# Kernel optimization log

Hardware: AMD Instinct MI355X
Metric: run time of the kernel (lower is better)

Reference implementation:

```python
import jax, jax.numpy as jnp
import numpy as np

D = 256; NH = 8; HD = D // NH; L = 4; P = 4; NQ = 900; BS = 8; DFFN = 1024
SHAPES = np.array([[128, 128], [64, 64], [32, 32], [16, 16]])  # (H, W) per level, static metadata
NV = int((SHAPES[:, 0] * SHAPES[:, 1]).sum())
EPS = 1e-6


def setup_inputs():
    key = jax.random.key(0)
    ks = iter(jax.random.split(key, 48))

    def nrm(shape, scale=0.02):
        return jax.random.normal(next(ks), shape, jnp.float32) * scale

    lsi = np.concatenate([[0], np.cumsum(SHAPES[:, 0] * SHAPES[:, 1])[:-1]]).astype(np.int64)
    return {
        'tgt': nrm((NQ, BS, D), 1.0),
        'tgt_query_pos': nrm((NQ, BS, D), 1.0),
        'tgt_reference_points': jax.random.uniform(next(ks), (NQ, BS, L, 2), jnp.float32),
        'memory': nrm((NV, BS, D), 1.0),
        'memory_spatial_shapes': jnp.asarray(SHAPES, jnp.int32),
        'memory_level_start_index': jnp.asarray(lsi, jnp.int32),
        'w_norm_sa': jnp.ones((D,), jnp.float32),
        'w_norm_ca': jnp.ones((D,), jnp.float32),
        'w_norm_ffn': jnp.ones((D,), jnp.float32),
        'ls_sa': jnp.full((D,), 1e-4, jnp.float32),
        'ls_ca': jnp.full((D,), 1e-4, jnp.float32),
        'ls_ffn': jnp.full((D,), 1e-4, jnp.float32),
        'Wq': nrm((D, D)), 'Wk': nrm((D, D)), 'Wv': nrm((D, D)),
        'bq': jnp.zeros((D,), jnp.float32), 'bk': jnp.zeros((D,), jnp.float32), 'bv': jnp.zeros((D,), jnp.float32),
        'Wo_sa': nrm((D, D)), 'bo_sa': jnp.zeros((D,), jnp.float32),
        'Wv_proj': nrm((D, D)), 'bv_proj': jnp.zeros((D,), jnp.float32),
        'W_off': nrm((NH * L * P * 2, D)), 'b_off': nrm((NH * L * P * 2,), 0.1),
        'W_attn': nrm((NH * L * P, D)), 'b_attn': jnp.zeros((NH * L * P,), jnp.float32),
        'W_out_ca': nrm((D, D)), 'bo_ca': jnp.zeros((D,), jnp.float32),
        'Wg': nrm((DFFN, D)), 'bg': jnp.zeros((DFFN,), jnp.float32),
        'Wu': nrm((DFFN, D)), 'bu': jnp.zeros((DFFN,), jnp.float32),
        'Wf': nrm((D, DFFN)), 'bf': jnp.zeros((D,), jnp.float32),
    }


def rmsnorm(x, w):
    return x * jax.lax.rsqrt(jnp.mean(x * x, axis=-1, keepdims=True) + EPS) * w


def ms_deform_sample(v, loc, attw):
    # v: (bs, nv, NH, HD); loc: (bs, nq, NH, L, P, 2) normalized (x, y); attw: (bs, nq, NH, L, P)
    bs, nq = loc.shape[0], loc.shape[1]
    out = jnp.zeros((bs, nq, NH, HD), loc.dtype)
    b_idx = jnp.arange(bs)[:, None, None, None]
    h_idx = jnp.arange(NH)[None, None, :, None]
    start = 0
    for l in range(L):
        Hl, Wl = int(SHAPES[l, 0]), int(SHAPES[l, 1])
        vf = v[:, start:start + Hl * Wl]  # (bs, Hl*Wl, NH, HD)
        start += Hl * Wl
        # grid_sample(align_corners=False, padding=zeros) pixel mapping
        x = loc[:, :, :, l, :, 0] * Wl - 0.5
        y = loc[:, :, :, l, :, 1] * Hl - 0.5
        x0 = jnp.floor(x)
        y0 = jnp.floor(y)
        acc = jnp.zeros((bs, nq, NH, P, HD), loc.dtype)
        for dx in (0, 1):
            for dy in (0, 1):
                xi = x0 + dx
                yi = y0 + dy
                w = (1.0 - jnp.abs(x - xi)) * (1.0 - jnp.abs(y - yi))
                valid = (xi >= 0) & (xi <= Wl - 1) & (yi >= 0) & (yi <= Hl - 1)
                w = jnp.where(valid, w, 0.0)
                idx = (jnp.clip(yi, 0, Hl - 1) * Wl + jnp.clip(xi, 0, Wl - 1)).astype(jnp.int32)
                acc = acc + w[..., None] * vf[b_idx, idx, h_idx]  # (bs, nq, NH, P, HD)
        out = out + jnp.einsum('bqhp,bqhpd->bqhd', attw[:, :, :, l], acc)
    return out


def reference(tgt, tgt_query_pos, tgt_reference_points, memory, memory_spatial_shapes,
              memory_level_start_index, w_norm_sa, w_norm_ca, w_norm_ffn, ls_sa, ls_ca, ls_ffn,
              Wq, Wk, Wv, bq, bk, bv, Wo_sa, bo_sa, Wv_proj, bv_proj, W_off, b_off, W_attn,
              b_attn, W_out_ca, bo_ca, Wg, bg, Wu, bu, Wf, bf):
    nq, bs, d = tgt.shape
    # --- self-attention (pre-norm + LayerScale residual) ---
    xn = rmsnorm(tgt, w_norm_sa)
    qk = xn + tgt_query_pos
    q = (qk @ Wq.T + bq).reshape(nq, bs, NH, HD)
    k = (qk @ Wk.T + bk).reshape(nq, bs, NH, HD)
    vv = (xn @ Wv.T + bv).reshape(nq, bs, NH, HD)
    scores = jnp.einsum('qbhd,kbhd->bhqk', q, k) * (1.0 / np.sqrt(HD))
    attn = jax.nn.softmax(scores, axis=-1)
    sa = jnp.einsum('bhqk,kbhd->qbhd', attn, vv).reshape(nq, bs, d) @ Wo_sa.T + bo_sa
    tgt = tgt + ls_sa * sa
    # --- multi-scale deformable cross-attention (identity=zeros in original) ---
    xn = rmsnorm(tgt, w_norm_ca)
    qca = jnp.swapaxes(xn + tgt_query_pos, 0, 1)  # (bs, nq, d)
    val = (jnp.swapaxes(memory, 0, 1) @ Wv_proj.T + bv_proj).reshape(bs, -1, NH, HD)
    off = (qca @ W_off.T + b_off).reshape(bs, nq, NH, L, P, 2)
    attw = jax.nn.softmax((qca @ W_attn.T + b_attn).reshape(bs, nq, NH, L * P), axis=-1)
    attw = attw.reshape(bs, nq, NH, L, P)
    norm = jnp.asarray(SHAPES[:, ::-1].copy(), jnp.float32)  # (W, H) per level
    ref = jnp.swapaxes(tgt_reference_points, 0, 1)  # (bs, nq, L, 2)
    loc = ref[:, :, None, :, None, :] + off / norm[None, None, None, :, None, :]
    ca = ms_deform_sample(val, loc, attw).reshape(bs, nq, d) @ W_out_ca.T + bo_ca
    tgt = tgt + ls_ca * jnp.swapaxes(ca, 0, 1)
    # --- SwiGLU FFN ---
    xn = rmsnorm(tgt, w_norm_ffn)
    ffn = (jax.nn.silu(xn @ Wg.T + bg) * (xn @ Wu.T + bu)) @ Wf.T + bf
    return tgt + ls_ffn * ffn
```

## Files before the change

kernel.cpp:

```cpp
#include <hip/hip_runtime.h>

typedef unsigned short ushort_t;
typedef unsigned int uint32;
typedef __bf16 bf16x8 __attribute__((ext_vector_type(8)));
typedef float f32x4 __attribute__((ext_vector_type(4)));
typedef ushort_t us4 __attribute__((ext_vector_type(4)));

#define D_    256
#define NH_   8
#define HD_   32
#define NQ_   900
#define BS_   8
#define TOK_  7200
#define NV_   21760
#define QP_   928
#define DFFN_ 1024

__device__ __forceinline__ ushort_t f2bf(float x) {
    union { float f; uint32 u; } v; v.f = x;
    uint32 r = v.u + 0x7FFFu + ((v.u >> 16) & 1u);
    return (ushort_t)(r >> 16);
}
__device__ __forceinline__ float bf2f(ushort_t h) {
    union { uint32 u; float f; } v; v.u = ((uint32)h) << 16;
    return v.f;
}
__device__ __forceinline__ int imin(int a, int b) { return a < b ? a : b; }
__device__ __forceinline__ int imax(int a, int b) { return a > b ? a : b; }

__global__ __launch_bounds__(256) void cvtall_k(
    const float* __restrict__ s0, const float* __restrict__ s1, const float* __restrict__ s2,
    const float* __restrict__ s3, const float* __restrict__ s4, const float* __restrict__ s5,
    const float* __restrict__ s6, const float* __restrict__ s7, const float* __restrict__ s8,
    const float* __restrict__ s9, const float* __restrict__ s10, ushort_t* __restrict__ dst,
    const float* __restrict__ bq, const float* __restrict__ bk,
    const float* __restrict__ boff, const float* __restrict__ battn,
    float* __restrict__ bias_qk, float* __restrict__ bias_ol) {
    int tid = threadIdx.x;
    if (blockIdx.x == 0) {
        bias_qk[tid] = bq[tid];
        bias_qk[256 + tid] = bk[tid];
        bias_ol[tid] = boff[tid];
        if (tid < 128) bias_ol[256 + tid] = battn[tid];
    }
    int id = blockIdx.x * 256 + tid;
    const float* s; int off;
    if      (id <  16384) { s = s0;  off = id; }
    else if (id <  32768) { s = s1;  off = id - 16384; }
    else if (id <  49152) { s = s2;  off = id - 32768; }
    else if (id <  65536) { s = s3;  off = id - 49152; }
    else if (id <  81920) { s = s4;  off = id - 65536; }
    else if (id <  98304) { s = s5;  off = id - 81920; }
    else if (id < 114688) { s = s6;  off = id - 98304; }
    else if (id < 122880) { s = s7;  off = id - 114688; }
    else if (id < 188416) { s = s8;  off = id - 122880; }
    else if (id < 253952) { s = s9;  off = id - 188416; }
    else                  { s = s10; off = id - 253952; }
    f32x4 v = *(const f32x4*)(s + (size_t)off * 4);
    us4 t;
#pragma unroll
    for (int e = 0; e < 4; e++) t[e] = f2bf(v[e]);
    *(us4*)(dst + (size_t)id * 4) = t;
}

__global__ __launch_bounds__(256) void rms_k(const float* __restrict__ x,
                                             const float* __restrict__ pos,
                                             const float* __restrict__ wn,
                                             ushort_t* __restrict__ xn_out,
                                             ushort_t* __restrict__ qk_out) {
    int r = blockIdx.x, tid = threadIdx.x;
    float v = x[r * D_ + tid];
    float ss = v * v;
#pragma unroll
    for (int o = 32; o; o >>= 1) ss += __shfl_xor(ss, o, 64);
    __shared__ float part[4];
    if ((tid & 63) == 0) part[tid >> 6] = ss;
    __syncthreads();
    float tot = part[0] + part[1] + part[2] + part[3];
    float sc = rsqrtf(tot * (1.f / 256.f) + 1e-6f);
    float xn = v * sc * wn[tid];
    if (xn_out) xn_out[r * D_ + tid] = f2bf(xn);
    if (qk_out) qk_out[r * D_ + tid] = f2bf(xn + pos[r * D_ + tid]);
}

enum { EPI_RESID, EPI_QK2, EPI_VT, EPI_VAL, EPI_OFFLOG };

template <int EPI, bool AF32, int BM, int BN, int WGM, int WGN, int TK>
__global__ __launch_bounds__(WGM * WGN * 64) void gemm2_k(
    const void* __restrict__ Ap, const ushort_t* __restrict__ Wp,
    const float* __restrict__ bias, void* __restrict__ outp, void* __restrict__ outp2,
    int M, int N, int swz,
    const float* __restrict__ resid, const float* __restrict__ ls, float scale) {
    constexpr int THREADS = WGM * WGN * 64;
    constexpr int NK  = TK / 32;
    constexpr int LDK = 40;
    constexpr int WR  = BM / WGM, WC = BN / WGN;
    constexpr int FM  = WR / 16,  FN = WC / 16;
    constexpr int ACH = AF32 ? (BM * 32 / 4 / THREADS) : (BM * 32 / 8 / THREADS);
    constexpr int BCH = BN * 32 / 8 / THREADS;

    __shared__ __align__(16) ushort_t As[2][BM * LDK];
    __shared__ __align__(16) ushort_t Bs[2][BN * LDK];

    const int tid = threadIdx.x, l = tid & 63, w = tid >> 6;
    const int wm = w % WGM, wn = w / WGM;
    int by = blockIdx.y;
    if (swz) { int cpx = gridDim.y >> 3; by = (by & 7) * cpx + (by >> 3); }
    const int m0 = by * BM, n0 = blockIdx.x * BN;
    const int lr = l & 15, lkb = (l >> 4) * 8;

    const ushort_t* Ab = (const ushort_t*)Ap;
    const float*    Af = (const float*)Ap;

    int aRow[ACH], aK[ACH], bRow[BCH], bK[BCH];
#pragma unroll
    for (int ch = 0; ch < ACH; ch++) {
        int cid = ch * THREADS + tid;
        if constexpr (AF32) { aRow[ch] = cid >> 3; aK[ch] = (cid & 7) * 4; }
        else                { aRow[ch] = cid >> 2; aK[ch] = (cid & 3) * 8; }
    }
#pragma unroll
    for (int ch = 0; ch < BCH; ch++) {
        int cid = ch * THREADS + tid;
        bRow[ch] = cid >> 2; bK[ch] = (cid & 3) * 8;
    }
    int aGRow[ACH];
#pragma unroll
    for (int ch = 0; ch < ACH; ch++) aGRow[ch] = imin(m0 + aRow[ch], M - 1);

    f32x4  aSTf[AF32 ? ACH : 1];
    bf16x8 aSTb[AF32 ? 1 : ACH];
    bf16x8 bST[BCH];

    auto load_regs = [&](int kt) {
        const int k0 = kt * 32;
#pragma unroll
        for (int ch = 0; ch < ACH; ch++) {
            if constexpr (AF32)
                aSTf[ch] = *(const f32x4*)(Af + (size_t)aGRow[ch] * TK + k0 + aK[ch]);
            else
                aSTb[ch] = *(const bf16x8*)(Ab + (size_t)aGRow[ch] * TK + k0 + aK[ch]);
        }
#pragma unroll
        for (int ch = 0; ch < BCH; ch++)
            bST[ch] = *(const bf16x8*)(Wp + (size_t)(n0 + bRow[ch]) * TK + k0 + bK[ch]);
    };
    auto write_lds = [&](int buf) {
#pragma unroll
        for (int ch = 0; ch < ACH; ch++) {
            if constexpr (AF32) {
                us4 t;
#pragma unroll
                for (int e = 0; e < 4; e++) t[e] = f2bf(aSTf[ch][e]);
                *(us4*)&As[buf][aRow[ch] * LDK + aK[ch]] = t;
            } else {
                *(bf16x8*)&As[buf][aRow[ch] * LDK + aK[ch]] = aSTb[ch];
            }
        }
#pragma unroll
        for (int ch = 0; ch < BCH; ch++)
            *(bf16x8*)&Bs[buf][bRow[ch] * LDK + bK[ch]] = bST[ch];
    };

    f32x4 acc[FM][FN];
#pragma unroll
    for (int i = 0; i < FM; i++)
#pragma unroll
        for (int j = 0; j < FN; j++) acc[i][j] = f32x4{0.f, 0.f, 0.f, 0.f};

    load_regs(0);
    write_lds(0);
    __syncthreads();

    for (int kt = 0; kt < NK; ++kt) {
        const int c = kt & 1;
        if (kt + 1 < NK) load_regs(kt + 1);

        bf16x8 af[FM], bf_[FN];
#pragma unroll
        for (int i = 0; i < FM; i++)
            af[i] = *(const bf16x8*)&As[c][(wm * WR + i * 16 + lr) * LDK + lkb];
#pragma unroll
        for (int j = 0; j < FN; j++)
            bf_[j] = *(const bf16x8*)&Bs[c][(wn * WC + j * 16 + lr) * LDK + lkb];
#pragma unroll
        for (int i = 0; i < FM; i++)
#pragma unroll
            for (int j = 0; j < FN; j++)
                acc[i][j] = __builtin_amdgcn_mfma_f32_16x16x32_bf16(af[i], bf_[j], acc[i][j], 0, 0, 0);

        if (kt + 1 < NK) write_lds(c ^ 1);
        __syncthreads();
    }

#pragma unroll
    for (int i = 0; i < FM; i++)
#pragma unroll
        for (int j = 0; j < FN; j++) {
            int col = n0 + wn * WC + j * 16 + lr;
            float bvv = bias[col];
#pragma unroll
            for (int e = 0; e < 4; e++) {
                int row = m0 + wm * WR + i * 16 + (l >> 4) * 4 + e;
                if (row >= M) continue;
                float v = acc[i][j][e] + bvv;
                if constexpr (EPI == EPI_RESID) {
                    size_t idx = (size_t)row * N + col;
                    ((float*)outp)[idx] = resid[idx] + ls[col] * v;
                } else if constexpr (EPI == EPI_QK2) {
                    int c2 = col & 255;
                    int q = row >> 3, bb = row & 7, h = c2 >> 5, hd = c2 & 31;
                    ushort_t* dst = (col < 256) ? (ushort_t*)outp : (ushort_t*)outp2;
                    float sc = (col < 256) ? scale : 1.f;
                    dst[((bb * NH_ + h) * QP_ + q) * HD_ + hd] = f2bf(v * sc);
                } else if constexpr (EPI == EPI_VT) {
                    int q = row >> 3, bb = row & 7, h = col >> 5, hd = col & 31;
                    ((ushort_t*)outp)[((bb * NH_ + h) * HD_ + hd) * QP_ + q] = f2bf(v);
                } else if constexpr (EPI == EPI_VAL) {
                    int vv = row >> 3, bb = row & 7, h = col >> 5, d = col & 31;
                    ((ushort_t*)outp)[(((size_t)(bb * NH_ + h)) * NV_ + vv) * HD_ + d] = f2bf(v);
                } else if constexpr (EPI == EPI_OFFLOG) {
                    if (col < 256) ((float*)outp)[(size_t)row * 256 + col] = v;
                    else           ((float*)outp2)[(size_t)row * 128 + col - 256] = v;
                }
            }
        }
}

__global__ __launch_bounds__(256) void ffn_k(
    const ushort_t* __restrict__ Ap, const ushort_t* __restrict__ Wg,
    const ushort_t* __restrict__ Wu, const float* __restrict__ bgp,
    const float* __restrict__ bup, ushort_t* __restrict__ outp, int M) {
    constexpr int BM = 64, BN = 128, TK = 256, NK = TK / 32, LDK = 40;
    constexpr int WR = 32, WC = 64, FM = 2, FN = 4;

    __shared__ __align__(16) ushort_t As[2][BM * LDK];
    __shared__ __align__(16) ushort_t Gs[2][BN * LDK];
    __shared__ __align__(16) ushort_t Us[2][BN * LDK];

    const int tid = threadIdx.x, l = tid & 63, w = tid >> 6;
    const int wm = w & 1, wn = w >> 1;
    const int m0 = blockIdx.y * BM, n0 = blockIdx.x * BN;
    const int lr = l & 15, lkb = (l >> 4) * 8;

    const int aRow = tid >> 2, aK = (tid & 3) * 8;
    int bRow[2], bK[2];
#pragma unroll
    for (int ch = 0; ch < 2; ch++) { int cid = ch * 256 + tid; bRow[ch] = cid >> 2; bK[ch] = (cid & 3) * 8; }
    const int aGRow = imin(m0 + aRow, M - 1);

    bf16x8 aST, gST[2], uST[2];
    auto load_regs = [&](int kt) {
        const int k0 = kt * 32;
        aST = *(const bf16x8*)(Ap + (size_t)aGRow * TK + k0 + aK);
#pragma unroll
        for (int ch = 0; ch < 2; ch++) {
            gST[ch] = *(const bf16x8*)(Wg + (size_t)(n0 + bRow[ch]) * TK + k0 + bK[ch]);
            uST[ch] = *(const bf16x8*)(Wu + (size_t)(n0 + bRow[ch]) * TK + k0 + bK[ch]);
        }
    };
    auto write_lds = [&](int buf) {
        *(bf16x8*)&As[buf][aRow * LDK + aK] = aST;
#pragma unroll
        for (int ch = 0; ch < 2; ch++) {
            *(bf16x8*)&Gs[buf][bRow[ch] * LDK + bK[ch]] = gST[ch];
            *(bf16x8*)&Us[buf][bRow[ch] * LDK + bK[ch]] = uST[ch];
        }
    };

    f32x4 accG[FM][FN], accU[FM][FN];
#pragma unroll
    for (int i = 0; i < FM; i++)
#pragma unroll
        for (int j = 0; j < FN; j++) { accG[i][j] = f32x4{0,0,0,0}; accU[i][j] = f32x4{0,0,0,0}; }

    load_regs(0);
    write_lds(0);
    __syncthreads();

    for (int kt = 0; kt < NK; ++kt) {
        const int c = kt & 1;
        if (kt + 1 < NK) load_regs(kt + 1);
        bf16x8 af[FM], gf[FN], uf[FN];
#pragma unroll
        for (int i = 0; i < FM; i++)
            af[i] = *(const bf16x8*)&As[c][(wm * WR + i * 16 + lr) * LDK + lkb];
#pragma unroll
        for (int j = 0; j < FN; j++) {
            gf[j] = *(const bf16x8*)&Gs[c][(wn * WC + j * 16 + lr) * LDK + lkb];
            uf[j] = *(const bf16x8*)&Us[c][(wn * WC + j * 16 + lr) * LDK + lkb];
        }
#pragma unroll
        for (int i = 0; i < FM; i++)
#pragma unroll
            for (int j = 0; j < FN; j++) {
                accG[i][j] = __builtin_amdgcn_mfma_f32_16x16x32_bf16(af[i], gf[j], accG[i][j], 0, 0, 0);
                accU[i][j] = __builtin_amdgcn_mfma_f32_16x16x32_bf16(af[i], uf[j], accU[i][j], 0, 0, 0);
            }
        if (kt + 1 < NK) write_lds(c ^ 1);
        __syncthreads();
    }

#pragma unroll
    for (int i = 0; i < FM; i++)
#pragma unroll
        for (int j = 0; j < FN; j++) {
            int col = n0 + wn * WC + j * 16 + lr;
            float bg_ = bgp[col], bu_ = bup[col];
#pragma unroll
            for (int e = 0; e < 4; e++) {
                int row = m0 + wm * WR + i * 16 + (l >> 4) * 4 + e;
                if (row >= M) continue;
                float g = accG[i][j][e] + bg_;
                float u = accU[i][j][e] + bu_;
                float s = g / (1.f + __expf(-g));
                outp[(size_t)row * DFFN_ + col] = f2bf(s * u);
            }
        }
}

__global__ __launch_bounds__(256) void attn2_k(const ushort_t* __restrict__ qb,
                                               const ushort_t* __restrict__ kb,
                                               const ushort_t* __restrict__ vtb,
                                               ushort_t* __restrict__ sab) {
    __shared__ __align__(16) ushort_t Pl[4][16 * 40];
    const int tid = threadIdx.x, l = tid & 63, w = tid >> 6;
    const int bh = blockIdx.y, b = bh >> 3, h = bh & 7;
    const int q0 = (blockIdx.x * 4 + w) * 16;
    if (q0 >= NQ_) return;
    const int q = l & 15, g = l >> 4;
    ushort_t* Pw = &Pl[w][0];

    const bf16x8 qf = *(const bf16x8*)(qb + ((size_t)bh * QP_ + q0 + q) * HD_ + g * 8);
    const ushort_t* kbase = kb + (size_t)bh * QP_ * HD_;
    const ushort_t* vbase = vtb + (size_t)bh * HD_ * QP_;

    f32x4 O0 = {0.f, 0.f, 0.f, 0.f}, O1 = {0.f, 0.f, 0.f, 0.f};
    float m = -1e30f, sl = 0.f;

    auto ldk = [&](int t, int u) {
        return *(const bf16x8*)(kbase + (size_t)(t * 32 + u * 16 + q) * HD_ + g * 8);
    };
    auto ldv = [&](int t, int dh) {
        return *(const bf16x8*)(vbase + (size_t)(dh * 16 + q) * QP_ + t * 32 + g * 8);
    };
    bf16x8 kA = ldk(0, 0), kB = ldk(0, 1), v0 = ldv(0, 0), v1 = ldv(0, 1);

    for (int t = 0; t < 29; ++t) {
        bf16x8 nkA, nkB, nv0, nv1;
        if (t < 28) { nkA = ldk(t + 1, 0); nkB = ldk(t + 1, 1); nv0 = ldv(t + 1, 0); nv1 = ldv(t + 1, 1); }
        const f32x4 z = {0.f, 0.f, 0.f, 0.f};
        f32x4 sA = __builtin_amdgcn_mfma_f32_16x16x32_bf16(kA, qf, z, 0, 0, 0);
        f32x4 sB = __builtin_amdgcn_mfma_f32_16x16x32_bf16(kB, qf, z, 0, 0, 0);
        if (t == 28) {
            int k0 = 896 + g * 4;
#pragma unroll
            for (int e = 0; e < 4; e++) {
                if (k0 + e >= NQ_)      sA[e] = -1e30f;
                if (k0 + 16 + e >= NQ_) sB[e] = -1e30f;
            }
        }
        float tm = fmaxf(fmaxf(fmaxf(sA[0], sA[1]), fmaxf(sA[2], sA[3])),
                         fmaxf(fmaxf(sB[0], sB[1]), fmaxf(sB[2], sB[3])));
        tm = fmaxf(tm, __shfl_xor(tm, 16, 64));
        tm = fmaxf(tm, __shfl_xor(tm, 32, 64));
        float mn = fmaxf(m, tm);
        float r = exp2f(m - mn);
        m = mn;
#pragma unroll
        for (int e = 0; e < 4; e++) { O0[e] *= r; O1[e] *= r; }
        float pA[4], pB[4], ps = 0.f;
#pragma unroll
        for (int e = 0; e < 4; e++) {
            pA[e] = exp2f(sA[e] - m); pB[e] = exp2f(sB[e] - m);
            ps += pA[e] + pB[e];
        }
        sl = sl * r + ps;
        uint32 a0, a1, b0, b1;
        asm("v_cvt_pk_bf16_f32 %0, %1, %2" : "=v"(a0) : "v"(pA[0]), "v"(pA[1]));
        asm("v_cvt_pk_bf16_f32 %0, %1, %2" : "=v"(a1) : "v"(pA[2]), "v"(pA[3]));
        asm("v_cvt_pk_bf16_f32 %0, %1, %2" : "=v"(b0) : "v"(pB[0]), "v"(pB[1]));
        asm("v_cvt_pk_bf16_f32 %0, %1, %2" : "=v"(b1) : "v"(pB[2]), "v"(pB[3]));
        { uint2 tt; tt.x = a0; tt.y = a1; *(uint2*)(Pw + q * 40 + g * 4) = tt; }
        { uint2 tt; tt.x = b0; tt.y = b1; *(uint2*)(Pw + q * 40 + 16 + g * 4) = tt; }
        bf16x8 pf = *(const bf16x8*)(Pw + q * 40 + g * 8);
        O0 = __builtin_amdgcn_mfma_f32_16x16x32_bf16(v0, pf, O0, 0, 0, 0);
        O1 = __builtin_amdgcn_mfma_f32_16x16x32_bf16(v1, pf, O1, 0, 0, 0);
        kA = nkA; kB = nkB; v0 = nv0; v1 = nv1;
    }

    sl += __shfl_xor(sl, 16, 64);
    sl += __shfl_xor(sl, 32, 64);
    float inv = 1.f / sl;
    int row_q = q0 + q;
    if (row_q < NQ_) {
        ushort_t* op = sab + ((size_t)row_q * BS_ + b) * D_ + h * HD_ + g * 4;
#pragma unroll
        for (int dh = 0; dh < 2; dh++) {
            f32x4 Ov = dh ? O1 : O0;
            float e0 = Ov[0] * inv, e1 = Ov[1] * inv, e2 = Ov[2] * inv, e3 = Ov[3] * inv;
            uint32 w0, w1;
            asm("v_cvt_pk_bf16_f32 %0, %1, %2" : "=v"(w0) : "v"(e0), "v"(e1));
            asm("v_cvt_pk_bf16_f32 %0, %1, %2" : "=v"(w1) : "v"(e2), "v"(e3));
            *(uint32*)(op + dh * 16) = w0;
            *(uint32*)(op + dh * 16 + 2) = w1;
        }
    }
}

__global__ __launch_bounds__(256) void deform_k(
    const float* __restrict__ offb, const float* __restrict__ logb,
    const float* __restrict__ refpts, const int* __restrict__ shapes,
    const int* __restrict__ lsi, const ushort_t* __restrict__ val,
    ushort_t* __restrict__ ca) {
    __shared__ float off_l[256];
    __shared__ float attw[128];
    const int r = blockIdx.x;
    const int b = r & 7;
    const int tid = threadIdx.x;

    off_l[tid] = offb[(size_t)r * 256 + tid];
    if (tid < 128) {
        float lg = logb[(size_t)r * 128 + tid];
        float m = lg;
#pragma unroll
        for (int o = 1; o < 16; o <<= 1) m = fmaxf(m, __shfl_xor(m, o, 16));
        float e = __expf(lg - m);
        float s = e;
#pragma unroll
        for (int o = 1; o < 16; o <<= 1) s += __shfl_xor(s, o, 16);
        attw[tid] = e / s;
    }
    __syncthreads();

    const int h = tid >> 5, d = tid & 31;
    const ushort_t* vb = val + ((size_t)(b * NH_ + h)) * NV_ * HD_;
    float acc = 0.f;
#pragma unroll
    for (int lvl = 0; lvl < 4; lvl++) {
        const int H = shapes[lvl * 2], W = shapes[lvl * 2 + 1];
        const int base = lsi[lvl];
        const float refx = refpts[(r * 4 + lvl) * 2];
        const float refy = refpts[(r * 4 + lvl) * 2 + 1];
#pragma unroll
        for (int p = 0; p < 4; p++) {
            int oi = ((h * 4 + lvl) * 4 + p) * 2;
            float x = (refx + off_l[oi] / (float)W) * (float)W - 0.5f;
            float y = (refy + off_l[oi + 1] / (float)H) * (float)H - 0.5f;
            float x0 = floorf(x), y0 = floorf(y);
            float fx = x - x0, fy = y - y0;
            int ix = (int)x0, iy = (int)y0;
            float sval = 0.f;
#pragma unroll
            for (int dy = 0; dy <= 1; dy++)
#pragma unroll
                for (int dx = 0; dx <= 1; dx++) {
                    int xi = ix + dx, yi = iy + dy;
                    float wq = (dx ? fx : 1.f - fx) * (dy ? fy : 1.f - fy);
                    if (xi < 0 || xi >= W || yi < 0 || yi >= H) wq = 0.f;
                    int cx = imin(imax(xi, 0), W - 1), cy = imin(imax(yi, 0), H - 1);
                    float vv = bf2f(vb[(size_t)(base + cy * W + cx) * HD_ + d]);
                    sval += wq * vv;
                }
            acc += attw[h * 16 + lvl * 4 + p] * sval;
        }
    }
    ca[(size_t)r * 256 + tid] = f2bf(acc);
}

extern "C" void kernel_launch(void* const* d_in, const int* in_sizes, int n_in,
                              void* d_out, int out_size, void* d_ws, size_t ws_size,
                              hipStream_t stream) {
    (void)in_sizes; (void)n_in; (void)out_size; (void)ws_size;
    const float* tgt    = (const float*)d_in[0];
    const float* qpos   = (const float*)d_in[1];
    const float* refp   = (const float*)d_in[2];
    const float* mem    = (const float*)d_in[3];
    const int*   shapes = (const int*)d_in[4];
    const int*   lsi    = (const int*)d_in[5];
    const float* wnsa   = (const float*)d_in[6];
    const float* wnca   = (const float*)d_in[7];
    const float* wnffn  = (const float*)d_in[8];
    const float* lssa   = (const float*)d_in[9];
    const float* lsca   = (const float*)d_in[10];
    const float* lsffn  = (const float*)d_in[11];
    const float* Wq = (const float*)d_in[12];
    const float* Wk = (const float*)d_in[13];
    const float* Wv = (const float*)d_in[14];
    const float* bq = (const float*)d_in[15];
    const float* bk = (const float*)d_in[16];
    const float* bvv = (const float*)d_in[17];
    const float* Wo_sa = (const float*)d_in[18];
    const float* bo_sa = (const float*)d_in[19];
    const float* Wv_proj = (const float*)d_in[20];
    const float* bv_proj = (const float*)d_in[21];
    const float* W_off = (const float*)d_in[22];
    const float* b_off = (const float*)d_in[23];
    const float* W_attn = (const float*)d_in[24];
    const float* b_attn = (const float*)d_in[25];
    const float* W_out = (const float*)d_in[26];
    const float* bo_ca = (const float*)d_in[27];
    const float* Wg = (const float*)d_in[28];
    const float* bg = (const float*)d_in[29];
    const float* Wu = (const float*)d_in[30];
    const float* bu = (const float*)d_in[31];
    const float* Wf = (const float*)d_in[32];
    const float* bff = (const float*)d_in[33];

    char* ws = (char*)d_ws;
    size_t o = 0;
    auto alloc = [&](size_t b) { size_t c = o; o += (b + 255) & ~(size_t)255; return c; };

    const size_t wq_o = alloc(65536 * 2), wk_o = alloc(65536 * 2), wv_o = alloc(65536 * 2);
    const size_t wosa_o = alloc(65536 * 2), wvp_o = alloc(65536 * 2), wout_o = alloc(65536 * 2);
    const size_t woff_o = alloc(65536 * 2), wattn_o = alloc(32768 * 2);
    const size_t wg_o = alloc(262144 * 2), wu_o = alloc(262144 * 2), wf_o = alloc(262144 * 2);
    const size_t bqk_o = alloc(512 * 4), bol_o = alloc(384 * 4);
    const size_t xnsa_o = alloc((size_t)TOK_ * D_ * 2);
    const size_t qksa_o = alloc((size_t)TOK_ * D_ * 2);
    const size_t qkvBytes = (size_t)BS_ * NH_ * QP_ * HD_ * 2;
    const size_t qb_o = alloc(qkvBytes);
    const size_t kb_o = alloc(qkvBytes);
    const size_t vt_o = alloc(qkvBytes + 512);
    const size_t sa_o = alloc((size_t)TOK_ * D_ * 2);
    const size_t tgt1_o = alloc((size_t)TOK_ * D_ * 4);
    const size_t qca_o = alloc((size_t)TOK_ * D_ * 2);
    const size_t offb_o = alloc((size_t)TOK_ * 256 * 4);
    const size_t logit_o = alloc((size_t)TOK_ * 128 * 4);
    const size_t ca_o = alloc((size_t)TOK_ * D_ * 2);
    const size_t tgt2_o = alloc((size_t)TOK_ * D_ * 4);
    const size_t val_o = alloc((size_t)NV_ * BS_ * D_ * 2);
    const size_t h_o  = val_o;
    const size_t xn3_o = h_o + (size_t)TOK_ * DFFN_ * 2;

    dim3 blk(256);
    cvtall_k<<<dim3(319488 / 256), blk, 0, stream>>>(
        Wq, Wk, Wv, Wo_sa, Wv_proj, W_out, W_off, W_attn, Wg, Wu, Wf,
        (ushort_t*)(ws + wq_o),
        bq, bk, b_off, b_attn, (float*)(ws + bqk_o), (float*)(ws + bol_o));

    (void)hipMemsetAsync(ws + vt_o, 0, qkvBytes + 512, stream);

    rms_k<<<dim3(TOK_), blk, 0, stream>>>(tgt, qpos, wnsa,
                                          (ushort_t*)(ws + xnsa_o), (ushort_t*)(ws + qksa_o));
    const float QSC = 0.25503321550239915f;
    gemm2_k<EPI_QK2, false, 64, 128, 2, 2, 256><<<dim3(4, 113), blk, 0, stream>>>(
        ws + qksa_o, (ushort_t*)(ws + wq_o), (const float*)(ws + bqk_o),
        ws + qb_o, ws + kb_o, TOK_, 512, 0, nullptr, nullptr, QSC);
    gemm2_k<EPI_VT, false, 64, 128, 2, 2, 256><<<dim3(2, 113), blk, 0, stream>>>(
        ws + xnsa_o, (ushort_t*)(ws + wv_o), bvv, ws + vt_o, nullptr, TOK_, 256, 0,
        nullptr, nullptr, 1.f);
    attn2_k<<<dim3(15, 64), blk, 0, stream>>>((ushort_t*)(ws + qb_o), (ushort_t*)(ws + kb_o),
                                              (ushort_t*)(ws + vt_o), (ushort_t*)(ws + sa_o));
    gemm2_k<EPI_RESID, false, 64, 128, 2, 2, 256><<<dim3(2, 113), blk, 0, stream>>>(
        ws + sa_o, (ushort_t*)(ws + wosa_o), bo_sa, ws + tgt1_o, nullptr, TOK_, 256, 0,
        tgt, lssa, 1.f);

    rms_k<<<dim3(TOK_), blk, 0, stream>>>((const float*)(ws + tgt1_o), qpos, wnca,
                                          nullptr, (ushort_t*)(ws + qca_o));
    gemm2_k<EPI_OFFLOG, false, 64, 128, 2, 2, 256><<<dim3(3, 113), blk, 0, stream>>>(
        ws + qca_o, (ushort_t*)(ws + woff_o), (const float*)(ws + bol_o),
        ws + offb_o, ws + logit_o, TOK_, 384, 0, nullptr, nullptr, 1.f);
    gemm2_k<EPI_VAL, true, 64, 256, 1, 4, 256><<<dim3(1, 2720), blk, 0, stream>>>(
        mem, (ushort_t*)(ws + wvp_o), bv_proj, ws + val_o, nullptr, NV_ * BS_, 256, 1,
        nullptr, nullptr, 1.f);
    deform_k<<<dim3(TOK_), blk, 0, stream>>>(
        (const float*)(ws + offb_o), (const float*)(ws + logit_o), refp, shapes, lsi,
        (ushort_t*)(ws + val_o), (ushort_t*)(ws + ca_o));
    gemm2_k<EPI_RESID, false, 64, 128, 2, 2, 256><<<dim3(2, 113), blk, 0, stream>>>(
        ws + ca_o, (ushort_t*)(ws + wout_o), bo_ca, ws + tgt2_o, nullptr, TOK_, 256, 0,
        (const float*)(ws + tgt1_o), lsca, 1.f);

    rms_k<<<dim3(TOK_), blk, 0, stream>>>((const float*)(ws + tgt2_o), nullptr, wnffn,
                                          (ushort_t*)(ws + xn3_o), nullptr);
    ffn_k<<<dim3(8, 113), blk, 0, stream>>>(
        (const ushort_t*)(ws + xn3_o), (const ushort_t*)(ws + wg_o),
        (const ushort_t*)(ws + wu_o), bg, bu, (ushort_t*)(ws + h_o), TOK_);
    gemm2_k<EPI_RESID, false, 64, 128, 2, 2, 1024><<<dim3(2, 113), blk, 0, stream>>>(
        ws + h_o, (ushort_t*)(ws + wf_o), bff, d_out, nullptr, TOK_, 256, 0,
        (const float*)(ws + tgt2_o), lsffn, 1.f);
}
```

Measured before the change: 365.7 us.

## Add dedicated value-projection GEMM keeping weight fragments in registers

Replaces the generic templated GEMM for the large memory value projection (M=174080, N=256, K=256) with a specialised kernel using 512 threads (8 waves), each wave owning 32 output columns. The B-operand (weights) is loaded straight from global memory into registers with prefetch, so only the fp32->bf16-converted A tile goes through shared memory. This cuts LDS traffic and shared memory use per block, which could raise occupancy. In exchange every wave re-reads weights from global/L2, and the scattered bf16 output write is unchanged.

```diff
diff --git a/kernel.cpp b/kernel.cpp
--- a/kernel.cpp
+++ b/kernel.cpp
@@ -83,7 +83,7 @@
     if (qk_out) qk_out[r * D_ + tid] = f2bf(xn + pos[r * D_ + tid]);
 }
 
-enum { EPI_RESID, EPI_QK2, EPI_VT, EPI_VAL, EPI_OFFLOG };
+enum { EPI_RESID, EPI_QK2, EPI_VT, EPI_OFFLOG };
 
 template <int EPI, bool AF32, int BM, int BN, int WGM, int WGN, int TK>
 __global__ __launch_bounds__(WGM * WGN * 64) void gemm2_k(
@@ -216,13 +216,86 @@
                 } else if constexpr (EPI == EPI_VT) {
                     int q = row >> 3, bb = row & 7, h = col >> 5, hd = col & 31;
                     ((ushort_t*)outp)[((bb * NH_ + h) * HD_ + hd) * QP_ + q] = f2bf(v);
-                } else if constexpr (EPI == EPI_VAL) {
-                    int vv = row >> 3, bb = row & 7, h = col >> 5, d = col & 31;
-                    ((ushort_t*)outp)[(((size_t)(bb * NH_ + h)) * NV_ + vv) * HD_ + d] = f2bf(v);
                 } else if constexpr (EPI == EPI_OFFLOG) {
                     if (col < 256) ((float*)outp)[(size_t)row * 256 + col] = v;
                     else           ((float*)outp2)[(size_t)row * 128 + col - 256] = v;
                 }
+            }
+        }
+}
+
+__global__ __launch_bounds__(512) void gemm4_k(
+    const float* __restrict__ Af, const ushort_t* __restrict__ Wp,
+    const float* __restrict__ bias, ushort_t* __restrict__ outp, int swz) {
+    constexpr int TK = 256, NK = 8, LDK = 40;
+    __shared__ __align__(16) ushort_t As[2][64 * LDK];
+
+    const int tid = threadIdx.x, l = tid & 63, w = tid >> 6;
+    int by = blockIdx.y;
+    if (swz) { int cpx = gridDim.y >> 3; by = (by & 7) * cpx + (by >> 3); }
+    const int m0 = by * 64;
+    const int lr = l & 15, g = l >> 4, lkb = g * 8;
+
+    const int aRow = tid >> 3, aK = (tid & 7) * 4;
+    const float* aPtr = Af + (size_t)(m0 + aRow) * TK + aK;
+    f32x4 aST;
+    auto loadA = [&](int kt) { aST = *(const f32x4*)(aPtr + kt * 32); };
+    auto writeA = [&](int buf) {
+        us4 t;
+#pragma unroll
+        for (int e = 0; e < 4; e++) t[e] = f2bf(aST[e]);
+        *(us4*)&As[buf][aRow * LDK + aK] = t;
+    };
+
+    const ushort_t* bPtr0 = Wp + (size_t)(w * 32 + lr) * TK + lkb;
+    const ushort_t* bPtr1 = Wp + (size_t)(w * 32 + 16 + lr) * TK + lkb;
+
+    f32x4 acc[4][2];
+#pragma unroll
+    for (int i = 0; i < 4; i++)
+#pragma unroll
+        for (int j = 0; j < 2; j++) acc[i][j] = f32x4{0.f, 0.f, 0.f, 0.f};
+
+    bf16x8 bC0, bC1, bN0, bN1;
+    loadA(0);
+    bC0 = *(const bf16x8*)(bPtr0);
+    bC1 = *(const bf16x8*)(bPtr1);
+    writeA(0);
+    __syncthreads();
+
+    for (int kt = 0; kt < NK; ++kt) {
+        const int c = kt & 1;
+        if (kt + 1 < NK) {
+            loadA(kt + 1);
+            bN0 = *(const bf16x8*)(bPtr0 + (kt + 1) * 32);
+            bN1 = *(const bf16x8*)(bPtr1 + (kt + 1) * 32);
+        }
+        bf16x8 af[4];
+#pragma unroll
+        for (int i = 0; i < 4; i++)
+            af[i] = *(const bf16x8*)&As[c][(i * 16 + lr) * LDK + lkb];
+#pragma unroll
+        for (int i = 0; i < 4; i++) {
+            acc[i][0] = __builtin_amdgcn_mfma_f32_16x16x32_bf16(af[i], bC0, acc[i][0], 0, 0, 0);
+            acc[i][1] = __builtin_amdgcn_mfma_f32_16x16x32_bf16(af[i], bC1, acc[i][1], 0, 0, 0);
+        }
+        if (kt + 1 < NK) writeA(c ^ 1);
+        __syncthreads();
+        bC0 = bN0; bC1 = bN1;
+    }
+
+#pragma unroll
+    for (int i = 0; i < 4; i++)
+#pragma unroll
+        for (int j = 0; j < 2; j++) {
+            int col = w * 32 + j * 16 + lr;
+            float bvv = bias[col];
+            int h = col >> 5, d = col & 31;
+#pragma unroll
+            for (int e = 0; e < 4; e++) {
+                int row = m0 + i * 16 + g * 4 + e;
+                int vv = row >> 3, bb = row & 7;
+                outp[(((size_t)(bb * NH_ + h)) * NV_ + vv) * HD_ + d] = f2bf(acc[i][j][e] + bvv);
             }
         }
 }
@@ -561,9 +634,8 @@
     gemm2_k<EPI_OFFLOG, false, 64, 128, 2, 2, 256><<<dim3(3, 113), blk, 0, stream>>>(
         ws + qca_o, (ushort_t*)(ws + woff_o), (const float*)(ws + bol_o),
         ws + offb_o, ws + logit_o, TOK_, 384, 0, nullptr, nullptr, 1.f);
-    gemm2_k<EPI_VAL, true, 64, 256, 1, 4, 256><<<dim3(1, 2720), blk, 0, stream>>>(
-        mem, (ushort_t*)(ws + wvp_o), bv_proj, ws + val_o, nullptr, NV_ * BS_, 256, 1,
-        nullptr, nullptr, 1.f);
+    gemm4_k<<<dim3(1, 2720), dim3(512), 0, stream>>>(
+        mem, (ushort_t*)(ws + wvp_o), bv_proj, (ushort_t*)(ws + val_o), 1);
     deform_k<<<dim3(TOK_), blk, 0, stream>>>(
         (const float*)(ws + offb_o), (const float*)(ws + logit_o), refp, shapes, lsi,
         (ushort_t*)(ws + val_o), (ushort_t*)(ws + ca_o));
```

After: 347.9 us. 4.9% less time.
